# Kernel optimization log

Hardware: AMD Instinct MI355X
Metric: run time of the kernel (lower is better)

The kernel has to match this reference:

```python
import jax, jax.numpy as jnp
import numpy as np

B, T, C, D = 8, 4096, 1024, 64  # batch, block_size, input_dim, output_dim


def setup_inputs() -> dict:
    key = jax.random.key(0)
    kx, kk, kq, kv = jax.random.split(key, 4)
    s = 1.0 / np.sqrt(C)  # nn.Linear default init range scale
    X = jax.random.normal(kx, (B, T, C), dtype=jnp.float32)
    Wk = jax.random.uniform(kk, (D, C), jnp.float32, -s, s) * 0.01  # key weight scaled by 0.01 per __post_init__
    Wq = jax.random.uniform(kq, (D, C), jnp.float32, -s, s)
    Wv = jax.random.uniform(kv, (D, C), jnp.float32, -s, s)
    return {"X": X, "Wk": Wk, "Wq": Wq, "Wv": Wv}


def reference(X, Wk, Wq, Wv):
    # bias-free linear projections (torch Linear: X @ W.T)
    keys = jnp.einsum('btc,dc->btd', X, Wk)
    queries = jnp.einsum('btc,dc->btd', X, Wq)
    values = jnp.einsum('btc,dc->btd', X, Wv)
    # scaled dot-product logits [B, T, T]
    logits = jnp.einsum('btd,bsd->bts', queries, keys) / jnp.sqrt(jnp.float32(D))
    causal = jnp.tril(jnp.ones((T, T), dtype=bool))
    logits = jnp.where(causal[None, :, :], logits, -jnp.inf)
    affinities = jax.nn.softmax(logits, axis=2)  # dropout_frac=0.0 -> identity
    return jnp.einsum('bts,bsd->btd', affinities, values)
```

## Files before the change

### kernel.cpp

```cpp
#include <hip/hip_runtime.h>


typedef short bf16x8 __attribute__((ext_vector_type(8)));
typedef short bf16x4 __attribute__((ext_vector_type(4)));
typedef float f32x4  __attribute__((ext_vector_type(4)));

static __device__ __forceinline__ short f2bf(float x) {
    union { float f; unsigned u; } v; v.f = x;
    return (short)((v.u + 0x7fffu + ((v.u >> 16) & 1u)) >> 16);
}

__global__ __launch_bounds__(64) void pack_w_kernel(
    const float* __restrict__ Wk, const float* __restrict__ Wq,
    const float* __restrict__ Wv, short* __restrict__ Wp)
{
    const int c    = blockIdx.x;
    const int lane = threadIdx.x;
    const int k2   = c & 1;
    const int m    = (c >> 1) % 3;
    const int ksw  = c / 6;
    const int ks   = ksw & 15;
    const int wq   = ksw >> 4;
    const int l15  = lane & 15;
    const int quad = lane >> 4;
    const float* W = (m == 0) ? Wk : (m == 1) ? Wq : Wv;
    const float sc = (m == 1) ? 0.18033688f : 1.0f;
    const float* p = W + (long)(wq * 16 + l15) * 1024 + ks * 64 + k2 * 32 + quad * 8;
    f32x4 a = *(const f32x4*)(p);
    f32x4 b = *(const f32x4*)(p + 4);
    bf16x8 f;
#pragma unroll
    for (int j = 0; j < 4; ++j) { f[j] = f2bf(a[j] * sc); f[j + 4] = f2bf(b[j] * sc); }
    *(bf16x8*)(Wp + (long)c * 512 + lane * 8) = f;
}

__global__ __launch_bounds__(256, 4) void proj_kernel(
    const float* __restrict__ X,
    const short* __restrict__ Wp,
    short* __restrict__ Kb,
    short* __restrict__ Qb,
    short* __restrict__ Vt)
{
    __shared__ __align__(16) short xs[2][32 * 72];
    const int tid  = threadIdx.x;
    const int w    = tid >> 6;
    const int lane = tid & 63;
    const int l15  = lane & 15;
    const int quad = lane >> 4;
    const int t0   = blockIdx.x * 32;

    const int rowA = tid >> 3, colg = tid & 7;
    const float* xpA = X + (long)(t0 + rowA) * 1024 + colg * 8;
    const int lwA = rowA * 72 + colg * 8;

    const short* wp = Wp + (long)(w * 16) * 6 * 512 + lane * 8;

    f32x4 acc[2][3];
#pragma unroll
    for (int rt = 0; rt < 2; ++rt)
#pragma unroll
        for (int m = 0; m < 3; ++m) { acc[rt][m][0]=0.f; acc[rt][m][1]=0.f; acc[rt][m][2]=0.f; acc[rt][m][3]=0.f; }

    f32x4 xr[2][2];
    bf16x8 wfc[3][2], wfn[3][2];

    {
#pragma unroll
        for (int s = 0; s < 2; ++s) {
            const int k0 = s * 64;
            xr[s][0] = *(const f32x4*)(xpA + k0);
            xr[s][1] = *(const f32x4*)(xpA + k0 + 4);
        }
#pragma unroll
        for (int m = 0; m < 3; ++m)
#pragma unroll
            for (int k2 = 0; k2 < 2; ++k2)
                wfc[m][k2] = *(const bf16x8*)(wp + (m * 2 + k2) * 512);
        bf16x8 c0;
#pragma unroll
        for (int j = 0; j < 4; ++j) { c0[j] = f2bf(xr[0][0][j]); c0[j+4] = f2bf(xr[0][1][j]); }
        *(bf16x8*)(&xs[0][lwA]) = c0;
    }
    __syncthreads();

#pragma unroll 2
    for (int ks = 0; ks < 16; ++ks) {
        const int buf = ks & 1;
        if (ks < 14) {
            const int k0 = (ks + 2) * 64;
            xr[buf][0] = *(const f32x4*)(xpA + k0);
            xr[buf][1] = *(const f32x4*)(xpA + k0 + 4);
        }
        if (ks < 15) {
            const int cb = (ks + 1) * 6;
#pragma unroll
            for (int m = 0; m < 3; ++m)
#pragma unroll
                for (int k2 = 0; k2 < 2; ++k2)
                    wfn[m][k2] = *(const bf16x8*)(wp + (cb + m * 2 + k2) * 512);
        }
#pragma unroll
        for (int k2 = 0; k2 < 2; ++k2)
#pragma unroll
            for (int rt = 0; rt < 2; ++rt) {
                bf16x8 a = *(const bf16x8*)(&xs[buf][(rt * 16 + l15) * 72 + k2 * 32 + quad * 8]);
#pragma unroll
                for (int m = 0; m < 3; ++m)
                    acc[rt][m] = __builtin_amdgcn_mfma_f32_16x16x32_bf16(a, wfc[m][k2], acc[rt][m], 0, 0, 0);
            }
        if (ks < 15) {
            const int nset = (ks + 1) & 1;
            bf16x8 c0;
#pragma unroll
            for (int j = 0; j < 4; ++j) { c0[j] = f2bf(xr[nset][0][j]); c0[j+4] = f2bf(xr[nset][1][j]); }
            *(bf16x8*)(&xs[nset][lwA]) = c0;
        }
        __syncthreads();
#pragma unroll
        for (int m = 0; m < 3; ++m)
#pragma unroll
            for (int k2 = 0; k2 < 2; ++k2) wfc[m][k2] = wfn[m][k2];
    }

    const int d    = w * 16 + l15;
    const int bidx = t0 >> 12;
#pragma unroll
    for (int rt = 0; rt < 2; ++rt) {
        const int tf = t0 + rt * 16 + quad * 4;
#pragma unroll
        for (int r = 0; r < 4; ++r) Kb[(long)(tf + r) * 64 + d] = f2bf(acc[rt][0][r]);
#pragma unroll
        for (int r = 0; r < 4; ++r) Qb[(long)(tf + r) * 64 + d] = f2bf(acc[rt][1][r]);
        bf16x4 pv;
#pragma unroll
        for (int r = 0; r < 4; ++r) pv[r] = f2bf(acc[rt][2][r]);
        *(bf16x4*)(Vt + ((long)bidx * 64 + d) * 4096 + (tf & 4095)) = pv;
    }
}

__global__ __launch_bounds__(256, 2) void flash_kernel(
    const short* __restrict__ Qb,
    const short* __restrict__ Kb,
    const short* __restrict__ Vt,
    float* __restrict__ Out)
{
    __shared__ __align__(16) char smem[33280];
    short* ps = (short*)smem;
    float* os = (float*)smem;
    float* ls = (float*)(smem + 32768);

    const int tid  = threadIdx.x;
    const int w    = tid >> 6;
    const int lane = tid & 63;
    const int l15  = lane & 15;
    const int quad = lane >> 4;
    const int b    = blockIdx.x & 7;
    const int tile = 127 - (blockIdx.x >> 3);
    const int t0   = tile * 32;

    const int nkb = (t0 >> 6) + 1;
    const int len = (nkb + 3) >> 2;
    const int kb0 = w * len;
    const int kb1 = (kb0 + len < nkb) ? (kb0 + len) : nkb;

    const short* Kbase = Kb + (long)b * 4096 * 64;
    const short* Vbase = Vt + (long)b * 64 * 4096;

    bf16x8 aq[2][2];
#pragma unroll
    for (int q2 = 0; q2 < 2; ++q2) {
        const long qoff = ((long)b * 4096 + t0 + q2 * 16 + l15) * 64;
        aq[q2][0] = *(const bf16x8*)(Qb + qoff + quad * 8);
        aq[q2][1] = *(const bf16x8*)(Qb + qoff + 32 + quad * 8);
    }

    bf16x8 bones;
#pragma unroll
    for (int j = 0; j < 8; ++j) bones[j] = (l15 == 0) ? (short)0x3F80 : (short)0;

    f32x4 o[2][4], lacc[2];
#pragma unroll
    for (int q2 = 0; q2 < 2; ++q2) {
        lacc[q2][0]=0.f; lacc[q2][1]=0.f; lacc[q2][2]=0.f; lacc[q2][3]=0.f;
#pragma unroll
        for (int dt = 0; dt < 4; ++dt) { o[q2][dt][0]=0.f; o[q2][dt][1]=0.f; o[q2][dt][2]=0.f; o[q2][dt][3]=0.f; }
    }

    bf16x8 kc[4][2], kn[4][2];
    if (kb0 < kb1) {
        const int s0 = kb0 << 6;
#pragma unroll
        for (int ct = 0; ct < 4; ++ct) {
            const short* kp = Kbase + (long)(s0 + ct * 16 + l15) * 64 + quad * 8;
            kc[ct][0] = *(const bf16x8*)(kp);
            kc[ct][1] = *(const bf16x8*)(kp + 32);
        }
    }

    for (int kb = kb0; kb < kb1; ++kb) {
        const int s0 = kb << 6;

        bf16x8 vf[4][2];
#pragma unroll
        for (int dt = 0; dt < 4; ++dt) {
            const short* vp = Vbase + (long)(dt * 16 + l15) * 4096 + s0 + quad * 8;
            vf[dt][0] = *(const bf16x8*)(vp);
            vf[dt][1] = *(const bf16x8*)(vp + 32);
        }
        if (kb + 1 < kb1) {
            const int sn = s0 + 64;
#pragma unroll
            for (int ct = 0; ct < 4; ++ct) {
                const short* kp = Kbase + (long)(sn + ct * 16 + l15) * 64 + quad * 8;
                kn[ct][0] = *(const bf16x8*)(kp);
                kn[ct][1] = *(const bf16x8*)(kp + 32);
            }
        }

#pragma unroll
        for (int q2 = 0; q2 < 2; ++q2) {
            short* myps = ps + ((w << 1) | q2) * 1152;
            f32x4 st[4];
#pragma unroll
            for (int ct = 0; ct < 4; ++ct) {
                f32x4 z; z[0]=0.f; z[1]=0.f; z[2]=0.f; z[3]=0.f;
                z = __builtin_amdgcn_mfma_f32_16x16x32_bf16(aq[q2][0], kc[ct][0], z, 0, 0, 0);
                st[ct] = __builtin_amdgcn_mfma_f32_16x16x32_bf16(aq[q2][1], kc[ct][1], st[ct] = z, 0, 0, 0);
            }
            if (kb == nkb - 1) {
#pragma unroll
                for (int ct = 0; ct < 4; ++ct) {
                    const int s = s0 + ct * 16 + l15;
#pragma unroll
                    for (int r = 0; r < 4; ++r)
                        if (s > t0 + q2 * 16 + quad * 4 + r) st[ct][r] = -1e30f;
                }
            }
#pragma unroll
            for (int ct = 0; ct < 4; ++ct)
#pragma unroll
                for (int r = 0; r < 4; ++r)
                    myps[(quad * 4 + r) * 72 + ct * 16 + l15] =
                        f2bf(__builtin_amdgcn_exp2f(st[ct][r]));
            bf16x8 ap0 = *(const bf16x8*)(myps + l15 * 72 + quad * 8);
            bf16x8 ap1 = *(const bf16x8*)(myps + l15 * 72 + 32 + quad * 8);
            lacc[q2] = __builtin_amdgcn_mfma_f32_16x16x32_bf16(ap0, bones, lacc[q2], 0, 0, 0);
            lacc[q2] = __builtin_amdgcn_mfma_f32_16x16x32_bf16(ap1, bones, lacc[q2], 0, 0, 0);
#pragma unroll
            for (int dt = 0; dt < 4; ++dt) {
                o[q2][dt] = __builtin_amdgcn_mfma_f32_16x16x32_bf16(ap0, vf[dt][0], o[q2][dt], 0, 0, 0);
                o[q2][dt] = __builtin_amdgcn_mfma_f32_16x16x32_bf16(ap1, vf[dt][1], o[q2][dt], 0, 0, 0);
            }
        }
#pragma unroll
        for (int ct = 0; ct < 4; ++ct) { kc[ct][0] = kn[ct][0]; kc[ct][1] = kn[ct][1]; }
    }

    __syncthreads();
#pragma unroll
    for (int q2 = 0; q2 < 2; ++q2) {
#pragma unroll
        for (int dt = 0; dt < 4; ++dt)
#pragma unroll
            for (int r = 0; r < 4; ++r)
                os[w * 2048 + (q2 * 16 + quad * 4 + r) * 64 + dt * 16 + l15] = o[q2][dt][r];
        if (l15 == 0) {
#pragma unroll
            for (int r = 0; r < 4; ++r) ls[w * 32 + q2 * 16 + quad * 4 + r] = lacc[q2][r];
        }
    }
    __syncthreads();

    const int row = tid >> 3, c0 = (tid & 7) * 8;
    f32x4 a0, a1; a0[0]=0.f;a0[1]=0.f;a0[2]=0.f;a0[3]=0.f; a1=a0;
    float lsum = 0.f;
#pragma unroll
    for (int w2 = 0; w2 < 4; ++w2) {
        f32x4 v0 = *(const f32x4*)(os + w2 * 2048 + row * 64 + c0);
        f32x4 v1 = *(const f32x4*)(os + w2 * 2048 + row * 64 + c0 + 4);
        a0[0]+=v0[0]; a0[1]+=v0[1]; a0[2]+=v0[2]; a0[3]+=v0[3];
        a1[0]+=v1[0]; a1[1]+=v1[1]; a1[2]+=v1[2]; a1[3]+=v1[3];
        lsum += ls[w2 * 32 + row];
    }
    const float inv = 1.0f / lsum;
    f32x4 r0, r1;
    r0[0]=a0[0]*inv; r0[1]=a0[1]*inv; r0[2]=a0[2]*inv; r0[3]=a0[3]*inv;
    r1[0]=a1[0]*inv; r1[1]=a1[1]*inv; r1[2]=a1[2]*inv; r1[3]=a1[3]*inv;
    float* op = Out + ((long)b * 4096 + t0 + row) * 64 + c0;
    *(f32x4*)(op)     = r0;
    *(f32x4*)(op + 4) = r1;
}

extern "C" void kernel_launch(void* const* d_in, const int* in_sizes, int n_in,
                              void* d_out, int out_size, void* d_ws, size_t ws_size,
                              hipStream_t stream) {
    const float* X  = (const float*)d_in[0];
    const float* Wk = (const float*)d_in[1];
    const float* Wq = (const float*)d_in[2];
    const float* Wv = (const float*)d_in[3];

    short* ws = (short*)d_ws;
    const long NE = (long)8 * 4096 * 64;
    short* Qb = ws;
    short* Kb = ws + NE;
    short* Vt = ws + 2 * NE;
    short* Wpk = ws + 3 * NE;

    pack_w_kernel<<<384, 64, 0, stream>>>(Wk, Wq, Wv, Wpk);
    proj_kernel<<<1024, 256, 0, stream>>>(X, Wpk, Kb, Qb, Vt);
    flash_kernel<<<1024, 256, 0, stream>>>(Qb, Kb, Vt, (float*)d_out);
}
```

Measured before the change: 279.2 us.

## Load X fragments directly into registers in projection kernel, drop LDS staging

The projection kernel no longer stages bf16-converted X tiles in shared memory with double buffering and barriers. Each wave now loads its MFMA A-fragments straight from global memory and converts them to bf16 in registers, with a one-step register prefetch over 32 half-steps. This removes LDS traffic and __syncthreads. In exchange, all four waves redundantly load and convert the same X rows, multiplying global/L2 reads of X by four, and each load is an uncoalesced per-lane fragment.

```diff
diff --git a/kernel.cpp b/kernel.cpp
--- a/kernel.cpp
+++ b/kernel.cpp
@@ -41,7 +41,6 @@
     short* __restrict__ Qb,
     short* __restrict__ Vt)
 {
-    __shared__ __align__(16) short xs[2][32 * 72];
     const int tid  = threadIdx.x;
     const int w    = tid >> 6;
     const int lane = tid & 63;
@@ -49,10 +48,8 @@
     const int quad = lane >> 4;
     const int t0   = blockIdx.x * 32;
 
-    const int rowA = tid >> 3, colg = tid & 7;
-    const float* xpA = X + (long)(t0 + rowA) * 1024 + colg * 8;
-    const int lwA = rowA * 72 + colg * 8;
-
+    const float* x0 = X + (long)(t0 + l15) * 1024 + quad * 8;
+    const float* x1 = x0 + 16 * 1024;
     const short* wp = Wp + (long)(w * 16) * 6 * 512 + lane * 8;
 
     f32x4 acc[2][3];
@@ -61,65 +58,44 @@
 #pragma unroll
         for (int m = 0; m < 3; ++m) { acc[rt][m][0]=0.f; acc[rt][m][1]=0.f; acc[rt][m][2]=0.f; acc[rt][m][3]=0.f; }
 
-    f32x4 xr[2][2];
-    bf16x8 wfc[3][2], wfn[3][2];
-
+    f32x4 xa, xb, xc, xd;
+    bf16x8 wc0, wc1, wc2;
     {
-#pragma unroll
-        for (int s = 0; s < 2; ++s) {
-            const int k0 = s * 64;
-            xr[s][0] = *(const f32x4*)(xpA + k0);
-            xr[s][1] = *(const f32x4*)(xpA + k0 + 4);
-        }
-#pragma unroll
-        for (int m = 0; m < 3; ++m)
-#pragma unroll
-            for (int k2 = 0; k2 < 2; ++k2)
-                wfc[m][k2] = *(const bf16x8*)(wp + (m * 2 + k2) * 512);
-        bf16x8 c0;
-#pragma unroll
-        for (int j = 0; j < 4; ++j) { c0[j] = f2bf(xr[0][0][j]); c0[j+4] = f2bf(xr[0][1][j]); }
-        *(bf16x8*)(&xs[0][lwA]) = c0;
-    }
-    __syncthreads();
-
-#pragma unroll 2
-    for (int ks = 0; ks < 16; ++ks) {
-        const int buf = ks & 1;
-        if (ks < 14) {
-            const int k0 = (ks + 2) * 64;
-            xr[buf][0] = *(const f32x4*)(xpA + k0);
-            xr[buf][1] = *(const f32x4*)(xpA + k0 + 4);
-        }
-        if (ks < 15) {
-            const int cb = (ks + 1) * 6;
-#pragma unroll
-            for (int m = 0; m < 3; ++m)
-#pragma unroll
-                for (int k2 = 0; k2 < 2; ++k2)
-                    wfn[m][k2] = *(const bf16x8*)(wp + (cb + m * 2 + k2) * 512);
-        }
-#pragma unroll
-        for (int k2 = 0; k2 < 2; ++k2)
-#pragma unroll
-            for (int rt = 0; rt < 2; ++rt) {
-                bf16x8 a = *(const bf16x8*)(&xs[buf][(rt * 16 + l15) * 72 + k2 * 32 + quad * 8]);
-#pragma unroll
-                for (int m = 0; m < 3; ++m)
-                    acc[rt][m] = __builtin_amdgcn_mfma_f32_16x16x32_bf16(a, wfc[m][k2], acc[rt][m], 0, 0, 0);
-            }
-        if (ks < 15) {
-            const int nset = (ks + 1) & 1;
-            bf16x8 c0;
-#pragma unroll
-            for (int j = 0; j < 4; ++j) { c0[j] = f2bf(xr[nset][0][j]); c0[j+4] = f2bf(xr[nset][1][j]); }
-            *(bf16x8*)(&xs[nset][lwA]) = c0;
-        }
-        __syncthreads();
-#pragma unroll
-        for (int m = 0; m < 3; ++m)
-#pragma unroll
-            for (int k2 = 0; k2 < 2; ++k2) wfc[m][k2] = wfn[m][k2];
+        xa = *(const f32x4*)(x0);     xb = *(const f32x4*)(x0 + 4);
+        xc = *(const f32x4*)(x1);     xd = *(const f32x4*)(x1 + 4);
+        wc0 = *(const bf16x8*)(wp);
+        wc1 = *(const bf16x8*)(wp + 2 * 512);
+        wc2 = *(const bf16x8*)(wp + 4 * 512);
+    }
+
+#pragma unroll
+    for (int hs = 0; hs < 32; ++hs) {
+        f32x4 na, nb, nc, nd;
+        bf16x8 wn0, wn1, wn2;
+        if (hs < 31) {
+            const int nks = (hs + 1) >> 1, nk2 = (hs + 1) & 1;
+            const int off = nks * 64 + nk2 * 32;
+            na = *(const f32x4*)(x0 + off);  nb = *(const f32x4*)(x0 + off + 4);
+            nc = *(const f32x4*)(x1 + off);  nd = *(const f32x4*)(x1 + off + 4);
+            const short* wb = wp + (size_t)(nks * 6 + nk2) * 512;
+            wn0 = *(const bf16x8*)(wb);
+            wn1 = *(const bf16x8*)(wb + 2 * 512);
+            wn2 = *(const bf16x8*)(wb + 4 * 512);
+        }
+        bf16x8 a0, a1;
+#pragma unroll
+        for (int j = 0; j < 4; ++j) {
+            a0[j] = f2bf(xa[j]); a0[j + 4] = f2bf(xb[j]);
+            a1[j] = f2bf(xc[j]); a1[j + 4] = f2bf(xd[j]);
+        }
+        acc[0][0] = __builtin_amdgcn_mfma_f32_16x16x32_bf16(a0, wc0, acc[0][0], 0, 0, 0);
+        acc[1][0] = __builtin_amdgcn_mfma_f32_16x16x32_bf16(a1, wc0, acc[1][0], 0, 0, 0);
+        acc[0][1] = __builtin_amdgcn_mfma_f32_16x16x32_bf16(a0, wc1, acc[0][1], 0, 0, 0);
+        acc[1][1] = __builtin_amdgcn_mfma_f32_16x16x32_bf16(a1, wc1, acc[1][1], 0, 0, 0);
+        acc[0][2] = __builtin_amdgcn_mfma_f32_16x16x32_bf16(a0, wc2, acc[0][2], 0, 0, 0);
+        acc[1][2] = __builtin_amdgcn_mfma_f32_16x16x32_bf16(a1, wc2, acc[1][2], 0, 0, 0);
+        xa = na; xb = nb; xc = nc; xd = nd;
+        wc0 = wn0; wc1 = wn1; wc2 = wn2;
     }
 
     const int d    = w * 16 + l15;
```

Result: slower. 332.9 us (+19.2%).
